# Kernel optimization log

Hardware: AMD Instinct MI355X
Metric: run time of the kernel (lower is better)

The kernel has to match this reference:

```python
import jax, jax.numpy as jnp
import numpy as np

NUM_GRAPHS = 4096
NODES_PER_GRAPH = 24
EDGES_PER_GRAPH = 48
LG_EDGES_PER_GRAPH = 144
N_ITER = 4
HID = 128
IN_DIM = 70
EDGE_DIM = 6


def seg_softmax(v, seg, num_seg):
    # numerically-stable softmax over segments; v: [E,1]
    m = jax.ops.segment_max(v, seg, num_segments=num_seg)
    e = jnp.exp(v - m[seg])
    s = jax.ops.segment_sum(e, seg, num_segments=num_seg)
    return e / s[seg]


def setup_inputs() -> dict:
    key = jax.random.key(0)
    ks = jax.random.split(key, 20)
    B, NPG, EPG, LPG = NUM_GRAPHS, NODES_PER_GRAPH, EDGES_PER_GRAPH, LG_EDGES_PER_GRAPH
    N, E, LE = B * NPG, B * EPG, B * LPG
    # graph-consistent random connectivity
    goff_n = (jnp.arange(B, dtype=jnp.int32) * NPG)[:, None]
    src = (goff_n + jax.random.randint(ks[0], (B, EPG), 0, NPG)).reshape(-1)
    dst = (goff_n + jax.random.randint(ks[1], (B, EPG), 0, NPG)).reshape(-1)
    edge_index = jnp.stack([src, dst]).astype(jnp.int32)
    goff_e = (jnp.arange(B, dtype=jnp.int32) * EPG)[:, None]
    lsrc = (goff_e + jax.random.randint(ks[2], (B, LPG), 0, EPG)).reshape(-1)
    ldst = (goff_e + jax.random.randint(ks[3], (B, LPG), 0, EPG)).reshape(-1)
    lg_edge_index = jnp.stack([lsrc, ldst]).astype(jnp.int32)
    edge_batch = jnp.repeat(jnp.arange(B, dtype=jnp.int32), EPG)
    s = 0.1
    inp = {
        "x": jax.random.normal(ks[4], (N, IN_DIM), jnp.float32),
        "edge_attr": jax.random.normal(ks[5], (E, EDGE_DIM), jnp.float32),
        "edge_index": edge_index,
        "lg_edge_index": lg_edge_index,
        "edge_batch": edge_batch,
        # params (stored [in, out] so we apply x @ W + b)
        "w_mlp": jax.random.normal(ks[6], (IN_DIM, HID), jnp.float32) * s,
        "b_mlp": jnp.zeros((HID,), jnp.float32),
        "w_u": jax.random.normal(ks[7], (HID, HID), jnp.float32) * s,
        "w_v": jax.random.normal(ks[8], (HID, HID), jnp.float32) * s,
        "w_edge": jax.random.normal(ks[9], (EDGE_DIM, HID), jnp.float32) * s,
        "w_rel": jax.random.normal(ks[10], (HID, 1), jnp.float32) * s,
        "b_rel": jnp.zeros((1,), jnp.float32),
        "w_root": jax.random.normal(ks[11], (HID, 1), jnp.float32) * s,
        "a": jax.random.normal(ks[12], (1, HID, N_ITER), jnp.float32) * s,
        "a_bias": jnp.zeros((1, 1, N_ITER), jnp.float32),
        "w_gout": jax.random.normal(ks[13], (HID, HID), jnp.float32) * s,
        "b_gout": jnp.zeros((HID,), jnp.float32),
        "w_block": jax.random.normal(ks[14], (HID, HID), jnp.float32) * s,
        "b_block": jnp.zeros((HID,), jnp.float32),
    }
    return inp


def reference(x, edge_attr, edge_index, lg_edge_index, edge_batch,
              w_mlp, b_mlp, w_u, w_v, w_edge, w_rel, b_rel, w_root,
              a, a_bias, w_gout, b_gout, w_block, b_block):
    N = x.shape[0]
    src, dst = edge_index[0], edge_index[1]
    lsrc, ldst = lg_edge_index[0], lg_edge_index[1]
    E = src.shape[0]

    # DrugEncoder.mlp
    h = x @ w_mlp + b_mlp  # [N, H]

    # initial directed-edge features: (lin_u(x)[src] + lin_v(x)[dst] + lin_edge(e)) / 3
    e0 = (h @ w_u)[src] + (h @ w_v)[dst] + edge_attr @ w_edge
    e0 = e0 / 3.0  # [E, H]

    out = e0
    outs, gouts = [], []
    for _ in range(N_ITER):
        # line-graph message passing: scatter-add over line-graph edges
        out = e0 + jax.ops.segment_sum(out[lsrc], ldst, num_segments=E)
        # GlobalAttentionPool: GraphConv(H->1) on the line graph, segment softmax, weighted add-pool
        aggr = jax.ops.segment_sum(out[lsrc], ldst, num_segments=E)
        xc = aggr @ w_rel + b_rel + out @ w_root  # [E, 1]
        sc = seg_softmax(xc, edge_batch, NUM_GRAPHS)  # [E, 1]
        g = jax.ops.segment_sum(out * sc, edge_batch, num_segments=NUM_GRAPHS)  # [B, H]
        outs.append(out)
        gouts.append(jnp.tanh(g @ w_gout + b_gout))

    out_all = jnp.stack(outs, axis=-1)    # [E, H, T]
    gout_all = jnp.stack(gouts, axis=-1)  # [B, H, T]

    # temporal attention over iterations
    scores = jnp.einsum('bht,ht->bt', gout_all, a[0])[:, None, :] + a_bias  # [B,1,T]
    scores = jax.nn.softmax(scores, axis=-1)
    per_edge = scores[edge_batch]  # gather == repeat_interleave by per-graph edge counts
    out = (out_all * per_edge).sum(-1)  # [E, H]

    # scatter edge features back to destination nodes
    xo = h + jax.ops.segment_sum(out, dst, num_segments=N)
    xo = xo @ w_block + b_block  # LinearBlock.lin1
    return xo
```

## Files before the change

kernel.cpp:

```cpp
#include <hip/hip_runtime.h>

#define NGR 4096
#define NPG 24
#define EPG 48
#define LPG 144
#define NITER 4
#define HID 128
#define NN (NGR*NPG)
#define NE (NGR*EPG)
#define NL (NGR*LPG)

typedef unsigned int uint;
typedef unsigned short ushort;
typedef short bf16x8 __attribute__((ext_vector_type(8)));
typedef unsigned short u16x4 __attribute__((ext_vector_type(4)));
typedef float f32x4 __attribute__((ext_vector_type(4)));
typedef float f32x2 __attribute__((ext_vector_type(2)));

__device__ __forceinline__ float b2f(ushort u){ return __uint_as_float(((uint)u)<<16); }
__device__ __forceinline__ ushort f2b(float f){
  uint x = __float_as_uint(f);
  x += 0x7FFFu + ((x>>16)&1u);
  return (ushort)(x>>16);
}
__device__ __forceinline__ float wredsum(float v){
  #pragma unroll
  for(int m=32;m;m>>=1) v += __shfl_xor(v, m, 64);
  return v;
}
__device__ __forceinline__ f32x4 mfma16(bf16x8 a, bf16x8 b, f32x4 c){
  return __builtin_amdgcn_mfma_f32_16x16x32_bf16(a, b, c, 0, 0, 0);
}

__global__ __launch_bounds__(256) void k_prep(
    const float* __restrict__ wmlp, const float* __restrict__ wu,
    const float* __restrict__ wv, const float* __restrict__ wb,
    ushort* __restrict__ P)
{
  int id = blockIdx.x*256 + threadIdx.x;
  if(id < 12288){
    int n=id/96, k=id-n*96;
    float v=(k<70)? wmlp[k*128+n] : 0.f;
    ushort hb=f2b(v); P[id]=hb; P[12288+id]=f2b(v-b2f(hb));
  } else if(id < 28672){
    int i=id-12288, n=i>>7, k=i&127;
    float v=wu[k*128+n]; ushort hb=f2b(v);
    P[24576+i]=hb; P[40960+i]=f2b(v-b2f(hb));
  } else if(id < 45056){
    int i=id-28672, n=i>>7, k=i&127;
    float v=wv[k*128+n]; ushort hb=f2b(v);
    P[57344+i]=hb; P[73728+i]=f2b(v-b2f(hb));
  } else if(id < 61440){
    int i=id-45056, n=i>>7, k=i&127;
    float v=wb[k*128+n]; ushort hb=f2b(v);
    P[90112+i]=hb; P[106496+i]=f2b(v-b2f(hb));
  }
}

__global__ __launch_bounds__(256,2) void k_fused(
  const float* __restrict__ x, const float* __restrict__ ea,
  const int* __restrict__ eidx, const int* __restrict__ lidx,
  const ushort* __restrict__ P,
  const float* __restrict__ bmlp, const float* __restrict__ wedge,
  const float* __restrict__ wrel, const float* __restrict__ brel,
  const float* __restrict__ wroot,
  const float* __restrict__ aatt, const float* __restrict__ abias,
  const float* __restrict__ wgout, const float* __restrict__ bgout,
  const float* __restrict__ bblock,
  float* __restrict__ out)
{
  const int g=blockIdx.x, tid=threadIdx.x, lane=tid&63, wid=tid>>6;
  const int q=lane>>4, ln=lane&15;
  const int E0=g*EPG, L0=g*LPG;
  const int nA = wid*32 + ln;

  __shared__ __align__(16) char LB[48320];
  ushort* Hh   = (ushort*)(LB + 0);
  ushort* Hl   = (ushort*)(LB + 6528);
  ushort* A_bf = (ushort*)(LB + 13056);
  ushort* OUTh = (ushort*)(LB + 18432);
  ushort* OUTl = (ushort*)(LB + 30720);
  ushort* A_cnt= (ushort*)(LB + 18432);
  ushort* xh   = (ushort*)(LB + 18432);
  ushort* xl   = (ushort*)(LB + 24576);
  float*  Pe   = (float*) (LB + 30720);
  float*  Re   = (float*) (LB + 30912);
  float*  eaL  = (float*) (LB + 31104);
  float*  nacc = (float*) (LB + 18432);
  int*    esrc = (int*)   (LB + 43008);
  int*    edst = (int*)   (LB + 43200);
  float*  xcs  = (float*) (LB + 43392);
  float*  gsf  = (float*) (LB + 44160);
  float*  sfull= (float*) (LB + 46208);
  float*  score= (float*) (LB + 48256);
  float*  wts  = (float*) (LB + 48272);
  float*  zeroF= (float*) (LB + 48288);

  const ushort *WmH=P, *WmL=P+12288, *WuH=P+24576, *WuL=P+40960,
               *WvH=P+57344, *WvL=P+73728, *WbH=P+90112, *WbL=P+106496;
  const f32x4 z4 = {0.f,0.f,0.f,0.f};

  f32x2 gxa[4];
  const f32x2* xg2 = (const f32x2*)(x + (size_t)g*NPG*70);
  #pragma unroll
  for(int i=0;i<4;i++){ int idx=tid+256*i; if(idx<840) gxa[i]=xg2[idx]; }
  for(int idx=tid; idx<1536; idx+=256) ((uint*)A_cnt)[idx]=0u;
  if(tid<48){
    int s=eidx[E0+tid]-g*NPG, d=eidx[NE+E0+tid]-g*NPG;
    esrc[tid]=s; edst[tid]=d; Pe[tid]=0.f; Re[tid]=0.f;
  }
  if(tid<8) zeroF[tid]=0.f;
  for(int idx=tid; idx<288; idx+=256) eaL[idx]=ea[(size_t)E0*6+idx];
  for(int idx=tid; idx<512; idx+=256) sfull[idx]=0.f;
  __syncthreads();
  if(tid<LPG){ int ls=lidx[L0+tid]-E0, ld=lidx[NL+L0+tid]-E0;
    atomicAdd(((uint*)A_cnt) + ((ld*64+ls)>>1), 1u<<((ls&1)*16)); }
  __syncthreads();
  for(int idx=tid; idx<48*48; idx+=256){ int i=idx/48, j=idx-i*48;
    A_bf[i*56+j]=f2b((float)A_cnt[i*64+j]); }
  __syncthreads();
  #pragma unroll
  for(int i=0;i<4;i++){ int idx=tid+256*i; if(idx<840){
    int r=idx/35, c0=2*(idx-r*35);
    float v0=gxa[i].x, v1=gxa[i].y;
    ushort h0=f2b(v0), h1=f2b(v1);
    xh[r*96+c0]=h0;   xl[r*96+c0]=f2b(v0-b2f(h0));
    xh[r*96+c0+1]=h1; xl[r*96+c0+1]=f2b(v1-b2f(h1)); } }
  for(int idx=tid; idx<624; idx+=256){ int r=idx/26, c=70+(idx-r*26);
    xh[r*96+c]=0; xl[r*96+c]=0; }
  __syncthreads();

  {
    f32x4 hc[2][2];
    #pragma unroll
    for(int mt=0;mt<2;mt++){ hc[mt][0]=z4; hc[mt][1]=z4; }
    #pragma unroll
    for(int kt=0; kt<3; kt++){
      int ko=kt*32+q*8;
      bf16x8 ah0=*(const bf16x8*)&xh[ln*96+ko];
      bf16x8 ah1=*(const bf16x8*)&xh[(16+ln)*96+ko];
      bf16x8 al0=*(const bf16x8*)&xl[ln*96+ko];
      bf16x8 al1=*(const bf16x8*)&xl[(16+ln)*96+ko];
      #pragma unroll
      for(int nt=0;nt<2;nt++){
        int nb=(nA+nt*16)*96+ko;
        bf16x8 bh=*(const bf16x8*)&WmH[nb];
        bf16x8 bl=*(const bf16x8*)&WmL[nb];
        hc[0][nt]=mfma16(ah0,bh,hc[0][nt]);
        hc[0][nt]=mfma16(al0,bh,hc[0][nt]);
        hc[0][nt]=mfma16(ah0,bl,hc[0][nt]);
        hc[1][nt]=mfma16(ah1,bh,hc[1][nt]);
        hc[1][nt]=mfma16(al1,bh,hc[1][nt]);
        hc[1][nt]=mfma16(ah1,bl,hc[1][nt]);
      }
    }
    float bm0=bmlp[nA], bm1=bmlp[nA+16];
    #pragma unroll
    for(int nt=0;nt<2;nt++){ float bb=nt?bm1:bm0; int col=nA+nt*16;
      #pragma unroll
      for(int mt=0;mt<2;mt++)
        #pragma unroll
        for(int r=0;r<4;r++){
          int row=mt*16+q*4+r;
          if(row<24){
            float hvv=hc[mt][nt][r]+bb;
            ushort hb=f2b(hvv);
            Hh[row*136+col]=hb; Hl[row*136+col]=f2b(hvv-b2f(hb));
          }
        }
    }
  }
  __syncthreads();

  f32x4 e0f[3][2];
  {
    int sgm[3], dgm[3];
    #pragma unroll
    for(int mt=0;mt<3;mt++){ sgm[mt]=esrc[mt*16+ln]; dgm[mt]=edst[mt*16+ln]; }
    #pragma unroll
    for(int mt=0;mt<3;mt++){ e0f[mt][0]=z4; e0f[mt][1]=z4; }
    #pragma unroll
    for(int kt=0;kt<4;kt++){
      int ko=kt*32+q*8;
      bf16x8 BuH[2],BuL[2],BvH[2],BvL[2];
      #pragma unroll
      for(int nt=0;nt<2;nt++){
        int nb=(nA+nt*16)*128+ko;
        BuH[nt]=*(const bf16x8*)&WuH[nb]; BuL[nt]=*(const bf16x8*)&WuL[nb];
        BvH[nt]=*(const bf16x8*)&WvH[nb]; BvL[nt]=*(const bf16x8*)&WvL[nb];
      }
      #pragma unroll
      for(int mt=0;mt<3;mt++){
        bf16x8 ash=*(const bf16x8*)&Hh[sgm[mt]*136+ko];
        bf16x8 asl=*(const bf16x8*)&Hl[sgm[mt]*136+ko];
        bf16x8 adh=*(const bf16x8*)&Hh[dgm[mt]*136+ko];
        bf16x8 adl=*(const bf16x8*)&Hl[dgm[mt]*136+ko];
        #pragma unroll
        for(int nt=0;nt<2;nt++){
          f32x4 acc=e0f[mt][nt];
          acc=mfma16(ash,BuH[nt],acc);
          acc=mfma16(asl,BuH[nt],acc);
          acc=mfma16(ash,BuL[nt],acc);
          acc=mfma16(adh,BvH[nt],acc);
          acc=mfma16(adl,BvH[nt],acc);
          acc=mfma16(adh,BvL[nt],acc);
          e0f[mt][nt]=acc;
        }
      }
    }
  }
  {
    const float wrel0=wrel[nA], wrel1=wrel[nA+16];
    const float wroot0=wroot[nA], wroot1=wroot[nA+16];
    float wed0[6],wed1[6];
    #pragma unroll
    for(int k=0;k<6;k++){ wed0[k]=wedge[k*128+nA]; wed1[k]=wedge[k*128+nA+16]; }
    #pragma unroll
    for(int mt=0;mt<3;mt++)
      #pragma unroll
      for(int r=0;r<4;r++){
        int m=mt*16+q*4+r;
        float v0=e0f[mt][0][r], v1=e0f[mt][1][r];
        #pragma unroll
        for(int k=0;k<6;k++){ float e=eaL[m*6+k]; v0+=e*wed0[k]; v1+=e*wed1[k]; }
        e0f[mt][0][r]=v0*(1.f/3.f);
        e0f[mt][1][r]=v1*(1.f/3.f);
      }
    #pragma unroll
    for(int mt=0;mt<3;mt++)
      #pragma unroll
      for(int r=0;r<4;r++){
        float pp=e0f[mt][0][r]*wrel0  + e0f[mt][1][r]*wrel1;
        float rr=e0f[mt][0][r]*wroot0 + e0f[mt][1][r]*wroot1;
        #pragma unroll
        for(int msk=1;msk<16;msk<<=1){ pp+=__shfl_xor(pp,msk,64); rr+=__shfl_xor(rr,msk,64); }
        if(ln==0){ atomicAdd(&Pe[mt*16+q*4+r],pp); atomicAdd(&Re[mt*16+q*4+r],rr); }
      }
  }
  __syncthreads();

  if(wid==0){
    const float brel_f=brel[0];
    const int arow=(lane<48)?lane:0;
    float pprev=(lane<48)?Pe[lane]:0.f;
    float rprev=(lane<48)?Re[lane]:0.f;
    const float pe_l=pprev, re_l=rprev;
    float rlast=rprev;
    #pragma unroll
    for(int t=1;t<=5;t++){
      float s=0.f, sr=0.f;
      for(int j=0;j<48;j++){
        float a=b2f(A_bf[arow*56+j]);
        float pj=__shfl(pprev,j,64);
        float rj=__shfl(rprev,j,64);
        s+=a*pj; sr+=a*rj;
      }
      s+=pe_l; sr+=re_l;
      if(t>=2){
        float xv = s - pe_l + rlast + brel_f;
        float v=(lane<48)?xv:-3.0e38f;
        float mx=v;
        #pragma unroll
        for(int msk=32;msk;msk>>=1) mx=fmaxf(mx,__shfl_xor(mx,msk,64));
        float e2=(lane<48)?__expf(v-mx):0.f;
        float ss=e2;
        #pragma unroll
        for(int msk=32;msk;msk>>=1) ss+=__shfl_xor(ss,msk,64);
        if(lane<48) xcs[(t-2)*48+lane]=e2/ss;
      }
      pprev=s; rprev=sr; rlast=sr;
    }
  }
  __syncthreads();

  #define STORE_SPLIT(n_, mt_, v_) {                                        \
    int b_ = (mt_)*2 + (q>>1);                                              \
    int off_ = (n_)*48 + ((b_ ^ (((n_)>>3)&1))<<3) + ((q&1)<<2);            \
    u16x4 hh_, ll_;                                                         \
    _Pragma("unroll")                                                       \
    for(int r_=0;r_<4;r_++){ ushort h_=f2b((v_)[r_]);                       \
      hh_[r_]=h_; ll_[r_]=f2b((v_)[r_]-b2f(h_)); }                          \
    *(u16x4*)&OUTh[off_]=hh_; *(u16x4*)&OUTl[off_]=ll_; }

  f32x4 Ocur[3][2];
  #pragma unroll
  for(int mt=0;mt<3;mt++)
    #pragma unroll
    for(int nt=0;nt<2;nt++){
      int n=nA+nt*16;
      STORE_SPLIT(n, mt, e0f[mt][nt]);
    }
  #pragma unroll 1
  for(int t=0;t<NITER;t++){
    #pragma unroll
    for(int nt=0;nt<2;nt++){
      int n=nA+nt*16, sw=(n>>3)&1, base=n*48;
      bf16x8 Bh0=*(const bf16x8*)&OUTh[base+((q^sw)<<3)];
      bf16x8 Bl0=*(const bf16x8*)&OUTl[base+((q^sw)<<3)];
      const ushort* ph1=(q<2)? &OUTh[base+(((4+q)^sw)<<3)] : (const ushort*)zeroF;
      const ushort* pl1=(q<2)? &OUTl[base+(((4+q)^sw)<<3)] : (const ushort*)zeroF;
      bf16x8 Bh1=*(const bf16x8*)ph1;
      bf16x8 Bl1=*(const bf16x8*)pl1;
      #pragma unroll
      for(int mt=0;mt<3;mt++){
        int ar=(mt*16+ln)*56;
        bf16x8 a0=*(const bf16x8*)&A_bf[ar+q*8];
        const ushort* pa1=(q<2)? &A_bf[ar+32+q*8] : (const ushort*)zeroF;
        bf16x8 a1=*(const bf16x8*)pa1;
        f32x4 acc=e0f[mt][nt];
        acc=mfma16(a0,Bh0,acc);
        acc=mfma16(a1,Bh1,acc);
        acc=mfma16(a0,Bl0,acc);
        acc=mfma16(a1,Bl1,acc);
        Ocur[mt][nt]=acc;
      }
      #pragma unroll
      for(int mt=0;mt<3;mt++) STORE_SPLIT(n, mt, Ocur[mt][nt]);
    }
    float gp0=0.f, gp1=0.f;
    #pragma unroll
    for(int mt=0;mt<3;mt++)
      #pragma unroll
      for(int r=0;r<4;r++){
        float xcv=xcs[t*48+mt*16+q*4+r];
        gp0+=xcv*Ocur[mt][0][r];
        gp1+=xcv*Ocur[mt][1][r];
      }
    gp0+=__shfl_xor(gp0,16,64); gp0+=__shfl_xor(gp0,32,64);
    gp1+=__shfl_xor(gp1,16,64); gp1+=__shfl_xor(gp1,32,64);
    if(q==0){ gsf[t*128+nA]=gp0; gsf[t*128+nA+16]=gp1; }
  }
  __syncthreads();

  {
    float p00=0,p01=0,p10=0,p11=0,p20=0,p21=0,p30=0,p31=0;
    int k0=wid*32;
    for(int kk=0;kk<32;kk++){
      int k=k0+kk;
      f32x2 w=((const f32x2*)wgout)[k*64+lane];
      float g0=gsf[k], g1=gsf[128+k], g2=gsf[256+k], g3=gsf[384+k];
      p00+=g0*w.x; p01+=g0*w.y;
      p10+=g1*w.x; p11+=g1*w.y;
      p20+=g2*w.x; p21+=g2*w.y;
      p30+=g3*w.x; p31+=g3*w.y;
    }
    atomicAdd(&sfull[2*lane],p00);     atomicAdd(&sfull[2*lane+1],p01);
    atomicAdd(&sfull[128+2*lane],p10); atomicAdd(&sfull[128+2*lane+1],p11);
    atomicAdd(&sfull[256+2*lane],p20); atomicAdd(&sfull[256+2*lane+1],p21);
    atomicAdd(&sfull[384+2*lane],p30); atomicAdd(&sfull[384+2*lane+1],p31);
  }
  __syncthreads();
  {
    int t=wid;
    float s0v=sfull[t*128+2*lane]  +bgout[2*lane];
    float s1v=sfull[t*128+2*lane+1]+bgout[2*lane+1];
    float v=tanhf(s0v)*aatt[(2*lane)*4+t]+tanhf(s1v)*aatt[(2*lane+1)*4+t];
    v=wredsum(v);
    if(lane==0) score[t]=v+abias[t];
  }
  __syncthreads();
  if(tid==0){
    float m=fmaxf(fmaxf(score[0],score[1]),fmaxf(score[2],score[3]));
    float e0v=__expf(score[0]-m), e1v=__expf(score[1]-m),
          e2v=__expf(score[2]-m), e3v=__expf(score[3]-m);
    float s=e0v+e1v+e2v+e3v;
    wts[0]=e0v/s; wts[1]=e1v/s; wts[2]=e2v/s; wts[3]=e3v/s;
  }
  __syncthreads();

  {
    const float cc4=wts[3], cc3=cc4+wts[2], cc2=cc3+wts[1];
    f32x4 Z[3][2];
    #pragma unroll
    for(int mt=0;mt<3;mt++)
      #pragma unroll
      for(int nt=0;nt<2;nt++){
        #pragma unroll
        for(int r=0;r<4;r++) Z[mt][nt][r]=cc4*e0f[mt][nt][r];
        int n=nA+nt*16;
        STORE_SPLIT(n, mt, Z[mt][nt]);
      }
    #pragma unroll 1
    for(int s=0;s<NITER;s++){
      const float ci = (s==0)?cc3:(s==1)?cc2:1.f;
      #pragma unroll
      for(int nt=0;nt<2;nt++){
        int n=nA+nt*16, sw=(n>>3)&1, base=n*48;
        bf16x8 Bh0=*(const bf16x8*)&OUTh[base+((q^sw)<<3)];
        bf16x8 Bl0=*(const bf16x8*)&OUTl[base+((q^sw)<<3)];
        const ushort* ph1=(q<2)? &OUTh[base+(((4+q)^sw)<<3)] : (const ushort*)zeroF;
        const ushort* pl1=(q<2)? &OUTl[base+(((4+q)^sw)<<3)] : (const ushort*)zeroF;
        bf16x8 Bh1=*(const bf16x8*)ph1;
        bf16x8 Bl1=*(const bf16x8*)pl1;
        #pragma unroll
        for(int mt=0;mt<3;mt++){
          int ar=(mt*16+ln)*56;
          bf16x8 a0=*(const bf16x8*)&A_bf[ar+q*8];
          const ushort* pa1=(q<2)? &A_bf[ar+32+q*8] : (const ushort*)zeroF;
          bf16x8 a1=*(const bf16x8*)pa1;
          f32x4 acc;
          #pragma unroll
          for(int r=0;r<4;r++) acc[r]=ci*e0f[mt][nt][r];
          acc=mfma16(a0,Bh0,acc);
          acc=mfma16(a1,Bh1,acc);
          acc=mfma16(a0,Bl0,acc);
          acc=mfma16(a1,Bl1,acc);
          Z[mt][nt]=acc;
        }
        if(s<NITER-1){
          #pragma unroll
          for(int mt=0;mt<3;mt++) STORE_SPLIT(n, mt, Z[mt][nt]);
        }
      }
    }
    __syncthreads();
    for(int idx=tid; idx<3072; idx+=256) nacc[idx]=0.f;
    __syncthreads();
    #pragma unroll
    for(int mt=0;mt<3;mt++)
      #pragma unroll
      for(int nt=0;nt<2;nt++){
        int ncol=nA+nt*16;
        #pragma unroll
        for(int r=0;r<4;r++){
          int dn=edst[mt*16+q*4+r];
          atomicAdd(&nacc[dn*128+ncol],Z[mt][nt][r]);
        }
      }
  }
  __syncthreads();
  for(int idx=tid; idx<24*128; idx+=256){
    int n=idx>>7, k=idx&127;
    float zv=b2f(Hh[n*136+k])+b2f(Hl[n*136+k])+nacc[idx];
    ushort hb=f2b(zv);
    Hh[n*136+k]=hb; Hl[n*136+k]=f2b(zv-b2f(hb));
  }
  __syncthreads();
  {
    f32x4 c4[2][2];
    c4[0][0]=z4; c4[0][1]=z4; c4[1][0]=z4; c4[1][1]=z4;
    #pragma unroll
    for(int kt=0;kt<4;kt++){
      int ko=kt*32+q*8;
      bf16x8 ah0=*(const bf16x8*)&Hh[ln*136+ko];
      bf16x8 ah1=*(const bf16x8*)&Hh[(16+ln)*136+ko];
      bf16x8 al0=*(const bf16x8*)&Hl[ln*136+ko];
      bf16x8 al1=*(const bf16x8*)&Hl[(16+ln)*136+ko];
      #pragma unroll
      for(int nt=0;nt<2;nt++){
        int nb=(nA+nt*16)*128+ko;
        bf16x8 bh=*(const bf16x8*)&WbH[nb];
        bf16x8 bl=*(const bf16x8*)&WbL[nb];
        c4[0][nt]=mfma16(ah0,bh,c4[0][nt]);
        c4[0][nt]=mfma16(al0,bh,c4[0][nt]);
        c4[0][nt]=mfma16(ah0,bl,c4[0][nt]);
        c4[1][nt]=mfma16(ah1,bh,c4[1][nt]);
        c4[1][nt]=mfma16(al1,bh,c4[1][nt]);
        c4[1][nt]=mfma16(ah1,bl,c4[1][nt]);
      }
    }
    float bb0=bblock[nA], bb1=bblock[nA+16];
    #pragma unroll
    for(int nt=0;nt<2;nt++){ float bbx=nt?bb1:bb0; int col=nA+nt*16;
      #pragma unroll
      for(int mt=0;mt<2;mt++)
        #pragma unroll
        for(int r=0;r<4;r++){
          int row=mt*16+q*4+r;
          if(row<24) out[(size_t)(g*NPG+row)*128+col]=c4[mt][nt][r]+bbx;
        }
    }
  }
  #undef STORE_SPLIT
}

extern "C" void kernel_launch(void* const* d_in, const int* in_sizes, int n_in,
                              void* d_out, int out_size, void* d_ws, size_t ws_size,
                              hipStream_t stream)
{
  (void)in_sizes; (void)n_in; (void)out_size; (void)ws_size;
  const float* x      = (const float*)d_in[0];
  const float* eattr  = (const float*)d_in[1];
  const int*   eidx   = (const int*)d_in[2];
  const int*   lidx   = (const int*)d_in[3];
  const float* wmlp   = (const float*)d_in[5];
  const float* bmlp   = (const float*)d_in[6];
  const float* wu     = (const float*)d_in[7];
  const float* wvv    = (const float*)d_in[8];
  const float* wedge  = (const float*)d_in[9];
  const float* wrel   = (const float*)d_in[10];
  const float* brel   = (const float*)d_in[11];
  const float* wroot  = (const float*)d_in[12];
  const float* aatt   = (const float*)d_in[13];
  const float* abias  = (const float*)d_in[14];
  const float* wgout  = (const float*)d_in[15];
  const float* bgout  = (const float*)d_in[16];
  const float* wblock = (const float*)d_in[17];
  const float* bblock = (const float*)d_in[18];

  ushort* P = (ushort*)d_ws;

  k_prep <<<240, 256, 0, stream>>>(wmlp, wu, wvv, wblock, P);
  k_fused<<<NGR, 256, 0, stream>>>(x, eattr, eidx, lidx, P,
                                   bmlp, wedge, wrel, brel, wroot,
                                   aatt, abias, wgout, bgout, bblock,
                                   (float*)d_out);
}
```

Baseline: 562.8 us.

## Keep per-iteration outputs in registers instead of recomputing weighted recurrence

The first iteration loop now saves its per-iteration edge features in registers (h0,h1,h2 plus the final Ocur). The temporal-attention weighted sum is then formed directly from them rather than re-running a second Horner-style recurrence of four MFMA passes through shared memory. This removes roughly half of the line-graph matmul work, the extra split stores and one barrier, and skips the final unneeded store in the first loop. The cost is 72 extra live float registers per thread, which may lower occupancy or cause spills.

```diff
diff --git a/kernel.cpp b/kernel.cpp
--- a/kernel.cpp
+++ b/kernel.cpp
@@ -123,9 +123,9 @@
   for(int i=0;i<4;i++){ int idx=tid+256*i; if(idx<840){
     int r=idx/35, c0=2*(idx-r*35);
     float v0=gxa[i].x, v1=gxa[i].y;
-    ushort h0=f2b(v0), h1=f2b(v1);
-    xh[r*96+c0]=h0;   xl[r*96+c0]=f2b(v0-b2f(h0));
-    xh[r*96+c0+1]=h1; xl[r*96+c0+1]=f2b(v1-b2f(h1)); } }
+    ushort h0v=f2b(v0), h1v=f2b(v1);
+    xh[r*96+c0]=h0v;   xl[r*96+c0]=f2b(v0-b2f(h0v));
+    xh[r*96+c0+1]=h1v; xl[r*96+c0+1]=f2b(v1-b2f(h1v)); } }
   for(int idx=tid; idx<624; idx+=256){ int r=idx/26, c=70+(idx-r*26);
     xh[r*96+c]=0; xl[r*96+c]=0; }
   __syncthreads();
@@ -283,6 +283,7 @@
     *(u16x4*)&OUTh[off_]=hh_; *(u16x4*)&OUTl[off_]=ll_; }
 
   f32x4 Ocur[3][2];
+  f32x4 h0[3][2], h1[3][2], h2[3][2];
   #pragma unroll
   for(int mt=0;mt<3;mt++)
     #pragma unroll
@@ -314,8 +315,20 @@
         acc=mfma16(a1,Bl1,acc);
         Ocur[mt][nt]=acc;
       }
-      #pragma unroll
-      for(int mt=0;mt<3;mt++) STORE_SPLIT(n, mt, Ocur[mt][nt]);
+      if(t<NITER-1){
+        #pragma unroll
+        for(int mt=0;mt<3;mt++) STORE_SPLIT(n, mt, Ocur[mt][nt]);
+      }
+    }
+    if(t==0){
+      #pragma unroll
+      for(int mt=0;mt<3;mt++){ h0[mt][0]=Ocur[mt][0]; h0[mt][1]=Ocur[mt][1]; }
+    } else if(t==1){
+      #pragma unroll
+      for(int mt=0;mt<3;mt++){ h1[mt][0]=Ocur[mt][0]; h1[mt][1]=Ocur[mt][1]; }
+    } else if(t==2){
+      #pragma unroll
+      for(int mt=0;mt<3;mt++){ h2[mt][0]=Ocur[mt][0]; h2[mt][1]=Ocur[mt][1]; }
     }
     float gp0=0.f, gp1=0.f;
     #pragma unroll
@@ -331,6 +344,8 @@
     if(q==0){ gsf[t*128+nA]=gp0; gsf[t*128+nA+16]=gp1; }
   }
   __syncthreads();
+
+  for(int idx=tid; idx<3072; idx+=256) nacc[idx]=0.f;
 
   {
     float p00=0,p01=0,p10=0,p11=0,p20=0,p21=0,p30=0,p31=0;
@@ -369,53 +384,7 @@
   __syncthreads();
 
   {
-    const float cc4=wts[3], cc3=cc4+wts[2], cc2=cc3+wts[1];
-    f32x4 Z[3][2];
-    #pragma unroll
-    for(int mt=0;mt<3;mt++)
-      #pragma unroll
-      for(int nt=0;nt<2;nt++){
-        #pragma unroll
-        for(int r=0;r<4;r++) Z[mt][nt][r]=cc4*e0f[mt][nt][r];
-        int n=nA+nt*16;
-        STORE_SPLIT(n, mt, Z[mt][nt]);
-      }
-    #pragma unroll 1
-    for(int s=0;s<NITER;s++){
-      const float ci = (s==0)?cc3:(s==1)?cc2:1.f;
-      #pragma unroll
-      for(int nt=0;nt<2;nt++){
-        int n=nA+nt*16, sw=(n>>3)&1, base=n*48;
-        bf16x8 Bh0=*(const bf16x8*)&OUTh[base+((q^sw)<<3)];
-        bf16x8 Bl0=*(const bf16x8*)&OUTl[base+((q^sw)<<3)];
-        const ushort* ph1=(q<2)? &OUTh[base+(((4+q)^sw)<<3)] : (const ushort*)zeroF;
-        const ushort* pl1=(q<2)? &OUTl[base+(((4+q)^sw)<<3)] : (const ushort*)zeroF;
-        bf16x8 Bh1=*(const bf16x8*)ph1;
-        bf16x8 Bl1=*(const bf16x8*)pl1;
-        #pragma unroll
-        for(int mt=0;mt<3;mt++){
-          int ar=(mt*16+ln)*56;
-          bf16x8 a0=*(const bf16x8*)&A_bf[ar+q*8];
-          const ushort* pa1=(q<2)? &A_bf[ar+32+q*8] : (const ushort*)zeroF;
-          bf16x8 a1=*(const bf16x8*)pa1;
-          f32x4 acc;
-          #pragma unroll
-          for(int r=0;r<4;r++) acc[r]=ci*e0f[mt][nt][r];
-          acc=mfma16(a0,Bh0,acc);
-          acc=mfma16(a1,Bh1,acc);
-          acc=mfma16(a0,Bl0,acc);
-          acc=mfma16(a1,Bl1,acc);
-          Z[mt][nt]=acc;
-        }
-        if(s<NITER-1){
-          #pragma unroll
-          for(int mt=0;mt<3;mt++) STORE_SPLIT(n, mt, Z[mt][nt]);
-        }
-      }
-    }
-    __syncthreads();
-    for(int idx=tid; idx<3072; idx+=256) nacc[idx]=0.f;
-    __syncthreads();
+    const float w1=wts[0], w2=wts[1], w3=wts[2], w4=wts[3];
     #pragma unroll
     for(int mt=0;mt<3;mt++)
       #pragma unroll
@@ -423,8 +392,10 @@
         int ncol=nA+nt*16;
         #pragma unroll
         for(int r=0;r<4;r++){
+          float wv=w1*h0[mt][nt][r]+w2*h1[mt][nt][r]
+                  +w3*h2[mt][nt][r]+w4*Ocur[mt][nt][r];
           int dn=edst[mt*16+q*4+r];
-          atomicAdd(&nacc[dn*128+ncol],Z[mt][nt][r]);
+          atomicAdd(&nacc[dn*128+ncol],wv);
         }
       }
   }
```

Result: faster. 532.9 us, median of 2 (-5.3%).
